# Kernel tuning notes

Measured on AMD Instinct MI355X. Metric: run time of the kernel, lower is better.

Reference implementation:

```python
import jax, jax.numpy as jnp
import numpy as np

ALPHA = 0.2        # LeakyReLU negative slope
NEG_INF = -9e15    # mask value used by the torch module


def setup_inputs() -> dict:
    key = jax.random.key(0)
    ks = jax.random.split(key, 7)
    B, T, N, Cin = 4, 12, 1024, 64
    Fout, Em = 64, 16
    x = jax.random.normal(ks[0], (B, T, N, Cin), dtype=jnp.float32)
    adj = jax.random.randint(ks[1], (N, N), 0, 2, dtype=jnp.int32)
    emb1 = jax.random.normal(ks[2], (N, Em), dtype=jnp.float32)
    emb2 = jax.random.normal(ks[3], (N, Em), dtype=jnp.float32)
    W = jax.random.normal(ks[4], (Cin, Fout), dtype=jnp.float32) * (1.0 / np.sqrt(Cin))
    a = jax.random.normal(ks[5], (2 * Fout, 1), dtype=jnp.float32) * 0.1
    a2 = jax.random.normal(ks[6], (2 * Em, 1), dtype=jnp.float32) * 0.1
    return {"x": x, "adj": adj, "emb1": emb1, "emb2": emb2, "W": W, "a": a, "a2": a2}


def reference(x, adj, emb1, emb2, W, a, a2):
    B, T, N, Cin = x.shape
    Fout = W.shape[1]
    Em = emb1.shape[1]
    # Linear projection, fold batch*time: Wh [BT, N, Fout]
    Wh = jnp.einsum('btnc,cf->btnf', x, W).reshape(B * T, N, Fout)
    # Additive attention scores from node features
    s1 = Wh @ a[:Fout, 0]          # [BT, N]
    s2 = Wh @ a[Fout:, 0]          # [BT, N]
    e1 = s1[:, :, None] + s2[:, None, :]   # [BT, N, N]
    # Additive scores from static embeddings (shared across batch*time)
    f1 = emb1 @ a2[:Em, 0]         # [N]
    f2 = emb2 @ a2[Em:, 0]         # [N]
    e2 = f1[:, None] + f2[None, :]          # [N, N]
    e = jax.nn.leaky_relu(e1 + e2[None, :, :], negative_slope=ALPHA)
    # Adjacency mask + row softmax (dropout is inference no-op)
    att = jnp.where(adj[None, :, :] > 0, e, jnp.float32(NEG_INF))
    att = jax.nn.softmax(att, axis=-1)
    h_prime = att @ Wh                       # [BT, N, Fout]
    return jax.nn.elu(h_prime.reshape(B, T, N, Fout))
```

## Files before the change

### kernel.cpp

```cpp
#include <hip/hip_runtime.h>
#include <hip/hip_bf16.h>
#include <math.h>

#define BT 48
#define N 1024
#define F 64
#define CIN 64
#define EM 16
#define LRELU_A 0.2f
#define L2E 1.4426950408889634f

typedef short bf16x8 __attribute__((ext_vector_type(8)));
typedef float f32x4  __attribute__((ext_vector_type(4)));
typedef unsigned int u32x4 __attribute__((ext_vector_type(4)));

__device__ __forceinline__ unsigned short f2bf(float f) {
    unsigned int u = __float_as_uint(f);
    return (unsigned short)((u + 0x7FFFu + ((u >> 16) & 1u)) >> 16);
}

__global__ __launch_bounds__(256) void k_proj_misc(
    const float* __restrict__ x, const float* __restrict__ W,
    const float* __restrict__ a,
    const int* __restrict__ adj,
    const float* __restrict__ emb1, const float* __restrict__ emb2,
    const float* __restrict__ a2,
    unsigned short* __restrict__ WhSw,
    float* __restrict__ s1, float* __restrict__ s2,
    unsigned int* __restrict__ adjBits,
    float* __restrict__ f1, float* __restrict__ f2)
{
    const int tid = threadIdx.x;
    const int b   = blockIdx.x;

    __shared__ __align__(16) float sx[64 * 64];
    __shared__ __align__(16) float sWT[64 * 68];
    __shared__ __align__(16) unsigned short sT[64 * 80];

    const int bt  = b >> 4;
    const int n0  = (b & 15) * 64;
    const size_t grow = (size_t)bt * N + n0;

    {
        const float4* xv = (const float4*)(x + grow * CIN);
        float4* sxv = (float4*)sx;
        for (int i = tid; i < 64 * CIN / 4; i += 256) sxv[i] = xv[i];
        for (int i = tid; i < CIN * F; i += 256)
            sWT[(i & 63) * 68 + (i >> 6)] = W[i];
    }
    __syncthreads();

    const int f = tid & 63;
    const int w = tid >> 6;
    const float a1 = a[f], a2c = a[F + f];

    float acc[16];
#pragma unroll
    for (int t = 0; t < 16; ++t) acc[t] = 0.f;

    for (int cb = 0; cb < CIN; cb += 4) {
        const float4 wv = *(const float4*)&sWT[f * 68 + cb];
#pragma unroll
        for (int t = 0; t < 16; ++t) {
            const float4 xv = *(const float4*)&sx[(w * 16 + t) * 64 + cb];
            acc[t] = fmaf(xv.x, wv.x, acc[t]);
            acc[t] = fmaf(xv.y, wv.y, acc[t]);
            acc[t] = fmaf(xv.z, wv.z, acc[t]);
            acc[t] = fmaf(xv.w, wv.w, acc[t]);
        }
    }

#pragma unroll
    for (int t = 0; t < 16; ++t) {
        float v1 = acc[t] * a1;
        float v2 = acc[t] * a2c;
#pragma unroll
        for (int off = 32; off >= 1; off >>= 1) {
            v1 += __shfl_xor(v1, off, 64);
            v2 += __shfl_xor(v2, off, 64);
        }
        if (f == 0) {
            s1[grow + w * 16 + t] = v1;
            s2[grow + w * 16 + t] = v2;
        }
        sT[f * 80 + w * 16 + t] = f2bf(acc[t]);
    }
    __syncthreads();

    {
        const int ff = tid >> 2, q = tid & 3;
        const int slot = (q + ff) & 3;
        const int nb0 = (b & 15) * 2;
#pragma unroll
        for (int nbL = 0; nbL < 2; ++nbL) {
            const size_t dst = ((size_t)(bt * 32 + nb0 + nbL) * 64 + ff) * 32 + slot * 8;
            *(uint4*)&WhSw[dst] = *(const uint4*)&sT[ff * 80 + nbL * 32 + q * 8];
        }
    }

    if (b < 128) {
        const int idx = b * 256 + tid;
        const int r = idx >> 5, w32 = idx & 31;
        const int* p = adj + (size_t)r * N + w32 * 32;
        unsigned int m = 0;
#pragma unroll
        for (int j = 0; j < 32; ++j) m |= (p[j] > 0 ? 1u : 0u) << j;
        adjBits[idx] = m;
    } else if (b < 132) {
        const int n = (b - 128) * 256 + tid;
        float v1 = 0.f, v2 = 0.f;
#pragma unroll
        for (int k = 0; k < EM; ++k) {
            v1 = fmaf(emb1[n * EM + k], a2[k], v1);
            v2 = fmaf(emb2[n * EM + k], a2[EM + k], v2);
        }
        f1[n] = v1; f2[n] = v2;
    }
}


#define PAIR(x1e, x1o, x2e, x2o, bit, dest) do {                           \
    const bool s0_ = (x1e) > T;                                            \
    const bool s1_ = (x1o) > T;                                            \
    float p0_ = (s0_ ? (x1e) : (x2e)) * (s0_ ? E1 : E2);                   \
    float p1_ = (s1_ ? (x1o) : (x2o)) * (s1_ ? E1 : E2);                   \
    p0_ = ((mb_ >> (bit)) & 1u) ? p0_ : 0.f;                               \
    p1_ = ((mb_ >> ((bit) + 1)) & 1u) ? p1_ : 0.f;                         \
    lsum += p0_ + p1_;                                                     \
    dest = __builtin_amdgcn_perm(__float_as_uint(p1_) + 0x8000u,           \
                                 __float_as_uint(p0_) + 0x8000u,           \
                                 0x07060302u);                             \
} while (0)

#define MAKE_ONE(ch, ks, Avar, abword) do {                                \
    const int jb_ = (ch) * 128 + (ks) * 32 + q * 8;                        \
    const float4 x1a_ = *(const float4*)&sX1[jb_];                         \
    const float4 x1b_ = *(const float4*)&sX1[jb_ + 4];                     \
    const float4 x2a_ = *(const float4*)&sX2[jb_];                         \
    const float4 x2b_ = *(const float4*)&sX2[jb_ + 4];                     \
    const unsigned int mb_ = ((abword) >> (q * 8)) & 0xFFu;                \
    unsigned int u0_, u1_, u2_, u3_;                                       \
    PAIR(x1a_.x, x1a_.y, x2a_.x, x2a_.y, 0, u0_);                          \
    PAIR(x1a_.z, x1a_.w, x2a_.z, x2a_.w, 2, u1_);                          \
    PAIR(x1b_.x, x1b_.y, x2b_.x, x2b_.y, 4, u2_);                          \
    PAIR(x1b_.z, x1b_.w, x2b_.z, x2b_.w, 6, u3_);                          \
    u32x4 av_; av_.x = u0_; av_.y = u1_; av_.z = u2_; av_.w = u3_;         \
    Avar = __builtin_bit_cast(bf16x8, av_);                                \
} while (0)

#define MAKE_AFR(ch, A0, A1, A2, A3) do {                                  \
    const uint4 ab_ = *(const uint4*)&abRow[(ch) * 4];                     \
    MAKE_ONE(ch, 0, A0, ab_.x);                                            \
    MAKE_ONE(ch, 1, A1, ab_.y);                                            \
    MAKE_ONE(ch, 2, A2, ab_.z);                                            \
    MAKE_ONE(ch, 3, A3, ab_.w);                                            \
} while (0)

#define MFMA_KS(ct, ks, Af) do {                                           \
    const bf16x8 bb_ = *(const bf16x8*)(src_ + (ks) * 4096 +               \
                        ((ct) * 16 + m15) * 64 + slotoff);                 \
    acc##ct = __builtin_amdgcn_mfma_f32_16x16x32_bf16(Af, bb_, acc##ct,    \
                                                      0, 0, 0);            \
} while (0)

#define MFMA_CT(ct, A0, A1, A2, A3) do {                                   \
    MFMA_KS(ct, 0, A0); MFMA_KS(ct, 1, A1);                                \
    MFMA_KS(ct, 2, A2); MFMA_KS(ct, 3, A3);                                \
} while (0)

#define MFMA_CHUNK(ch, A0, A1, A2, A3) do {                                \
    const char* src_ = (const char*)sB[(ch) & 1];                          \
    MFMA_CT(0, A0, A1, A2, A3); MFMA_CT(1, A0, A1, A2, A3);                \
    MFMA_CT(2, A0, A1, A2, A3); MFMA_CT(3, A0, A1, A2, A3);                \
} while (0)

#define DMA(ch) do {                                                       \
    const unsigned short* dsrc_ = gBbt + (ch) * 8192 + w * 2048 + lane * 8;\
    unsigned short* ddst_ = &sB[(ch) & 1][w * 2048];                       \
    __builtin_amdgcn_global_load_lds(                                      \
        (const __attribute__((address_space(1))) unsigned int*)(dsrc_),    \
        (__attribute__((address_space(3))) unsigned int*)(ddst_), 16, 0, 0);\
    __builtin_amdgcn_global_load_lds(                                      \
        (const __attribute__((address_space(1))) unsigned int*)(dsrc_+512),\
        (__attribute__((address_space(3))) unsigned int*)(ddst_+512), 16, 0, 0);\
    __builtin_amdgcn_global_load_lds(                                      \
        (const __attribute__((address_space(1))) unsigned int*)(dsrc_+1024),\
        (__attribute__((address_space(3))) unsigned int*)(ddst_+1024), 16, 0, 0);\
    __builtin_amdgcn_global_load_lds(                                      \
        (const __attribute__((address_space(1))) unsigned int*)(dsrc_+1536),\
        (__attribute__((address_space(3))) unsigned int*)(ddst_+1536), 16, 0, 0);\
} while (0)

#define EPI(ct, accv) do {                                                 \
    float h0_ = accv.x * rinv0, h1_ = accv.y * rinv1,                      \
          h2_ = accv.z * rinv2, h3_ = accv.w * rinv3;                      \
    h0_ = (h0_ > 0.f) ? h0_ : (__expf(h0_) - 1.f);                         \
    h1_ = (h1_ > 0.f) ? h1_ : (__expf(h1_) - 1.f);                         \
    h2_ = (h2_ > 0.f) ? h2_ : (__expf(h2_) - 1.f);                         \
    h3_ = (h3_ > 0.f) ? h3_ : (__expf(h3_) - 1.f);                         \
    float* op_ = out + (size_t)(bt * N + i0 + w * 16 + q * 4) * F          \
                 + (ct) * 16 + m15;                                        \
    op_[0 * F] = h0_; op_[1 * F] = h1_; op_[2 * F] = h2_; op_[3 * F] = h3_;\
} while (0)

__global__ __launch_bounds__(256, 3) void k_attn(
    const unsigned int* __restrict__ adjBits,
    const unsigned short* __restrict__ WhSw,
    const float* __restrict__ s1, const float* __restrict__ s2,
    const float* __restrict__ f1v, const float* __restrict__ f2v,
    float* __restrict__ out)
{
    __shared__ __align__(16) float sX1[N];
    __shared__ __align__(16) float sX2[N];
    __shared__ __align__(16) unsigned short sB[2][8192];
    __shared__ float sWmax[4];

    const int tid  = threadIdx.x;
    const int xcd = blockIdx.x & 7;
    const int idx = blockIdx.x >> 3;
    const int bt  = xcd * 6 + (idx >> 4);
    const int i0  = (idx & 15) * 64;
    const int lane = tid & 63;
    const int w    = tid >> 6;
    const int q    = lane >> 4;
    const int m15  = lane & 15;

    float cmax = -1e30f;
    for (int j = tid; j < N; j += 256) {
        const float c = (s2[bt * N + j] + f2v[j]) * L2E;
        sX1[j] = exp2f(c);
        sX2[j] = exp2f(LRELU_A * c);
        cmax = fmaxf(cmax, c);
    }
#pragma unroll
    for (int off = 32; off >= 1; off >>= 1) cmax = fmaxf(cmax, __shfl_xor(cmax, off, 64));
    if (lane == 0) sWmax[w] = cmax;
    __syncthreads();
    const float mx = fmaxf(fmaxf(sWmax[0], sWmax[1]), fmaxf(sWmax[2], sWmax[3]));

    const int growq = i0 + w * 16 + m15;
    const float r    = (s1[bt * N + growq] + f1v[growq]) * L2E;
    const float smx  = r + mx;
    const float mhat = fmaxf(smx, LRELU_A * smx);
    const float E1 = exp2f(r - mhat);
    const float E2 = exp2f(LRELU_A * r - mhat);
    const float T  = exp2f(-r);
    float lsum = 0.f;

    const unsigned int* abRow = adjBits + growq * 32;
    const unsigned short* gBbt = WhSw + (size_t)bt * 65536;
    const int slotoff = ((q + m15) & 3) * 16;

    f32x4 acc0 = 0.f, acc1 = 0.f, acc2 = 0.f, acc3 = 0.f;
    bf16x8 fA0, fA1, fA2, fA3, fB0, fB1, fB2, fB3;

    DMA(0);
    MAKE_AFR(0, fA0, fA1, fA2, fA3);
    __syncthreads();

    DMA(1); MFMA_CHUNK(0, fA0, fA1, fA2, fA3); MAKE_AFR(1, fB0, fB1, fB2, fB3); __syncthreads();
    DMA(2); MFMA_CHUNK(1, fB0, fB1, fB2, fB3); MAKE_AFR(2, fA0, fA1, fA2, fA3); __syncthreads();
    DMA(3); MFMA_CHUNK(2, fA0, fA1, fA2, fA3); MAKE_AFR(3, fB0, fB1, fB2, fB3); __syncthreads();
    DMA(4); MFMA_CHUNK(3, fB0, fB1, fB2, fB3); MAKE_AFR(4, fA0, fA1, fA2, fA3); __syncthreads();
    DMA(5); MFMA_CHUNK(4, fA0, fA1, fA2, fA3); MAKE_AFR(5, fB0, fB1, fB2, fB3); __syncthreads();
    DMA(6); MFMA_CHUNK(5, fB0, fB1, fB2, fB3); MAKE_AFR(6, fA0, fA1, fA2, fA3); __syncthreads();
    DMA(7); MFMA_CHUNK(6, fA0, fA1, fA2, fA3); MAKE_AFR(7, fB0, fB1, fB2, fB3); __syncthreads();
    MFMA_CHUNK(7, fB0, fB1, fB2, fB3);

    lsum += __shfl_xor(lsum, 16, 64);
    lsum += __shfl_xor(lsum, 32, 64);

    const float rinv0 = 1.f / __shfl(lsum, q * 4 + 0, 64);
    const float rinv1 = 1.f / __shfl(lsum, q * 4 + 1, 64);
    const float rinv2 = 1.f / __shfl(lsum, q * 4 + 2, 64);
    const float rinv3 = 1.f / __shfl(lsum, q * 4 + 3, 64);

    EPI(0, acc0); EPI(1, acc1); EPI(2, acc2); EPI(3, acc3);
}

extern "C" void kernel_launch(void* const* d_in, const int* in_sizes, int n_in,
                              void* d_out, int out_size, void* d_ws, size_t ws_size,
                              hipStream_t stream)
{
    const float* x    = (const float*)d_in[0];
    const int*   adj  = (const int*)  d_in[1];
    const float* emb1 = (const float*)d_in[2];
    const float* emb2 = (const float*)d_in[3];
    const float* W    = (const float*)d_in[4];
    const float* a    = (const float*)d_in[5];
    const float* a2   = (const float*)d_in[6];
    float* out = (float*)d_out;

    unsigned short* WhSw = (unsigned short*)d_ws;
    float* s1 = (float*)(WhSw + (size_t)BT * 65536);
    float* s2 = s1 + BT * N;
    float* f1 = s2 + BT * N;
    float* f2 = f1 + N;
    unsigned int* adjBits = (unsigned int*)(f2 + N);

    hipLaunchKernelGGL(k_proj_misc, dim3(768), dim3(256), 0, stream,
                       x, W, a, adj, emb1, emb2, a2, WhSw, s1, s2, adjBits, f1, f2);
    hipLaunchKernelGGL(k_attn, dim3(BT * 16), dim3(256), 0, stream,
                       adjBits, WhSw, s1, s2, f1, f2, out);
}
```

Measured before the change: 118.3 us.

## Deepen LDS DMA pipeline with explicit vmcnt waits and hoist adjacency loads

Loads all eight adjacency-bit words and the row score at kernel start, so their latency overlaps the column-exponent prologue instead of sitting on the main loop. The chunk loop now keeps two global-to-LDS transfers in flight. It waits with explicit s_waitcnt vmcnt counts and raw s_barrier instead of __syncthreads, so the next chunk's loads overlap the current chunk's MFMA work. The risk is that correctness depends on the assumed number of outstanding loads per DMA call. Extra live registers for the prefetched adjacency words could also reduce occupancy.

Measured after the change: 118.5 us. Within noise of the previous version (+0.1%).

```diff
diff --git a/kernel.cpp b/kernel.cpp
--- a/kernel.cpp
+++ b/kernel.cpp
@@ -118,6 +118,10 @@
     }
 }
 
+
+#define WAIT_VM4 asm volatile("s_waitcnt vmcnt(4)" ::: "memory")
+#define WAIT_VM0 asm volatile("s_waitcnt vmcnt(0)" ::: "memory")
+#define BAR __builtin_amdgcn_s_barrier()
 
 #define PAIR(x1e, x1o, x2e, x2o, bit, dest) do {                           \
     const bool s0_ = (x1e) > T;                                            \
@@ -148,12 +152,11 @@
     Avar = __builtin_bit_cast(bf16x8, av_);                                \
 } while (0)
 
-#define MAKE_AFR(ch, A0, A1, A2, A3) do {                                  \
-    const uint4 ab_ = *(const uint4*)&abRow[(ch) * 4];                     \
-    MAKE_ONE(ch, 0, A0, ab_.x);                                            \
-    MAKE_ONE(ch, 1, A1, ab_.y);                                            \
-    MAKE_ONE(ch, 2, A2, ab_.z);                                            \
-    MAKE_ONE(ch, 3, A3, ab_.w);                                            \
+#define MAKE_AFR(ch, abv, A0, A1, A2, A3) do {                             \
+    MAKE_ONE(ch, 0, A0, abv.x);                                            \
+    MAKE_ONE(ch, 1, A1, abv.y);                                            \
+    MAKE_ONE(ch, 2, A2, abv.z);                                            \
+    MAKE_ONE(ch, 3, A3, abv.w);                                            \
 } while (0)
 
 #define MFMA_KS(ct, ks, Af) do {                                           \
@@ -225,6 +228,14 @@
     const int q    = lane >> 4;
     const int m15  = lane & 15;
 
+    const int growq = i0 + w * 16 + m15;
+    const unsigned int* abRow = adjBits + growq * 32;
+    const uint4* abRow4 = (const uint4*)abRow;
+
+    const uint4 ab0 = abRow4[0], ab1 = abRow4[1], ab2 = abRow4[2], ab3 = abRow4[3];
+    const uint4 ab4 = abRow4[4], ab5 = abRow4[5], ab6 = abRow4[6], ab7 = abRow4[7];
+    const float rraw = s1[bt * N + growq] + f1v[growq];
+
     float cmax = -1e30f;
     for (int j = tid; j < N; j += 256) {
         const float c = (s2[bt * N + j] + f2v[j]) * L2E;
@@ -238,8 +249,7 @@
     __syncthreads();
     const float mx = fmaxf(fmaxf(sWmax[0], sWmax[1]), fmaxf(sWmax[2], sWmax[3]));
 
-    const int growq = i0 + w * 16 + m15;
-    const float r    = (s1[bt * N + growq] + f1v[growq]) * L2E;
+    const float r    = rraw * L2E;
     const float smx  = r + mx;
     const float mhat = fmaxf(smx, LRELU_A * smx);
     const float E1 = exp2f(r - mhat);
@@ -247,24 +257,30 @@
     const float T  = exp2f(-r);
     float lsum = 0.f;
 
-    const unsigned int* abRow = adjBits + growq * 32;
     const unsigned short* gBbt = WhSw + (size_t)bt * 65536;
     const int slotoff = ((q + m15) & 3) * 16;
 
     f32x4 acc0 = 0.f, acc1 = 0.f, acc2 = 0.f, acc3 = 0.f;
     bf16x8 fA0, fA1, fA2, fA3, fB0, fB1, fB2, fB3;
 
-    DMA(0);
-    MAKE_AFR(0, fA0, fA1, fA2, fA3);
-    __syncthreads();
-
-    DMA(1); MFMA_CHUNK(0, fA0, fA1, fA2, fA3); MAKE_AFR(1, fB0, fB1, fB2, fB3); __syncthreads();
-    DMA(2); MFMA_CHUNK(1, fB0, fB1, fB2, fB3); MAKE_AFR(2, fA0, fA1, fA2, fA3); __syncthreads();
-    DMA(3); MFMA_CHUNK(2, fA0, fA1, fA2, fA3); MAKE_AFR(3, fB0, fB1, fB2, fB3); __syncthreads();
-    DMA(4); MFMA_CHUNK(3, fB0, fB1, fB2, fB3); MAKE_AFR(4, fA0, fA1, fA2, fA3); __syncthreads();
-    DMA(5); MFMA_CHUNK(4, fA0, fA1, fA2, fA3); MAKE_AFR(5, fB0, fB1, fB2, fB3); __syncthreads();
-    DMA(6); MFMA_CHUNK(5, fB0, fB1, fB2, fB3); MAKE_AFR(6, fA0, fA1, fA2, fA3); __syncthreads();
-    DMA(7); MFMA_CHUNK(6, fA0, fA1, fA2, fA3); MAKE_AFR(7, fB0, fB1, fB2, fB3); __syncthreads();
+    MAKE_AFR(0, ab0, fA0, fA1, fA2, fA3);
+    DMA(0); DMA(1);
+
+    WAIT_VM4; BAR;
+    MFMA_CHUNK(0, fA0, fA1, fA2, fA3); MAKE_AFR(1, ab1, fB0, fB1, fB2, fB3);
+    BAR; DMA(2); WAIT_VM4; BAR;
+    MFMA_CHUNK(1, fB0, fB1, fB2, fB3); MAKE_AFR(2, ab2, fA0, fA1, fA2, fA3);
+    BAR; DMA(3); WAIT_VM4; BAR;
+    MFMA_CHUNK(2, fA0, fA1, fA2, fA3); MAKE_AFR(3, ab3, fB0, fB1, fB2, fB3);
+    BAR; DMA(4); WAIT_VM4; BAR;
+    MFMA_CHUNK(3, fB0, fB1, fB2, fB3); MAKE_AFR(4, ab4, fA0, fA1, fA2, fA3);
+    BAR; DMA(5); WAIT_VM4; BAR;
+    MFMA_CHUNK(4, fA0, fA1, fA2, fA3); MAKE_AFR(5, ab5, fB0, fB1, fB2, fB3);
+    BAR; DMA(6); WAIT_VM4; BAR;
+    MFMA_CHUNK(5, fB0, fB1, fB2, fB3); MAKE_AFR(6, ab6, fA0, fA1, fA2, fA3);
+    BAR; DMA(7); WAIT_VM4; BAR;
+    MFMA_CHUNK(6, fA0, fA1, fA2, fA3); MAKE_AFR(7, ab7, fB0, fB1, fB2, fB3);
+    WAIT_VM0; BAR;
     MFMA_CHUNK(7, fB0, fB1, fB2, fB3);
 
     lsum += __shfl_xor(lsum, 16, 64);
```
